# Kernel tuning notes

Hardware: AMD Instinct MI355X
Metric: run time of the kernel (lower is better)

Reference implementation:

```python
import jax, jax.numpy as jnp
import numpy as np

D_MODEL = 512
NHEAD = 8
COORD_DIM = 3
B, N = 2, 2048


def setup_inputs() -> dict:
    key = jax.random.key(0)
    ks = jax.random.split(key, 6)
    x = jax.random.normal(ks[0], (B, N, D_MODEL), dtype=jnp.float32)
    coords = jax.random.normal(ks[1], (B, N, COORD_DIM), dtype=jnp.float32)
    attn_mask = jax.random.normal(ks[2], (N, N), dtype=jnp.float32)
    # qkv Linear(d_model, 3*d_model) with bias
    lim = 1.0 / np.sqrt(D_MODEL)
    qkv_w = jax.random.uniform(ks[3], (3 * D_MODEL, D_MODEL), dtype=jnp.float32, minval=-lim, maxval=lim)
    qkv_b = jax.random.uniform(ks[4], (3 * D_MODEL,), dtype=jnp.float32, minval=-lim, maxval=lim)
    # rel_weight is zeros-init in torch; use small random values for a nontrivial test
    rel_weight = 0.02 * jax.random.normal(ks[5], (NHEAD, COORD_DIM), dtype=jnp.float32)
    return {"x": x, "coords": coords, "attn_mask": attn_mask,
            "qkv_w": qkv_w, "qkv_b": qkv_b, "rel_weight": rel_weight}


def reference(x, coords, attn_mask, qkv_w, qkv_b, rel_weight):
    Bb, Nn, D = x.shape
    H = rel_weight.shape[0]
    hd = D // H
    scale = 1.0 / jnp.sqrt(jnp.asarray(hd, dtype=x.dtype))

    qkv = x @ qkv_w.T + qkv_b                      # [B,N,3D]
    q, k, v = jnp.split(qkv, 3, axis=-1)

    def to_heads(t):
        return t.reshape(Bb, Nn, H, hd).transpose(0, 2, 1, 3)  # [B,H,N,hd]

    qh, kh, vh = to_heads(q), to_heads(k), to_heads(v)

    # per-head scalar projection of coordinates: [B,H,N]
    coord_proj = jnp.einsum('bnc,hc->bhn', coords.astype(jnp.float32), rel_weight).astype(x.dtype)

    # scores with relative-coordinate bias and additive float mask (2d kind)
    scores = jnp.einsum('bhqd,bhkd->bhqk', qh, kh) * scale
    scores = scores + coord_proj[:, :, :, None] - coord_proj[:, :, None, :]
    scores = scores + attn_mask[None, None, :, :]

    attn = jax.nn.softmax(scores, axis=-1)
    yh = jnp.einsum('bhqk,bhkd->bhqd', attn, vh)   # [B,H,N,hd]
    return yh.transpose(0, 2, 1, 3).reshape(Bb, Nn, D)
```

## Files before the change

kernel.cpp:

```cpp
#include <hip/hip_runtime.h>
#include <hip/hip_bf16.h>

typedef __bf16 bf16;
typedef __bf16 bf16x4 __attribute__((ext_vector_type(4)));
typedef __bf16 bf16x8 __attribute__((ext_vector_type(8)));
typedef float floatx4 __attribute__((ext_vector_type(4)));

#define D_MODEL 512
#define NHEAD 8
#define HD 64
#define NB 2
#define NN 2048
#define BH (NB*NHEAD)
#define LOG2E 1.4426950408889634f

__global__ __launch_bounds__(256) void convxw(const float* __restrict__ x,
                                              const float* __restrict__ w,
                                              const float* __restrict__ coords,
                                              const float* __restrict__ rw,
                                              bf16* __restrict__ xb,
                                              bf16* __restrict__ wb,
                                              float* __restrict__ cp) {
    int bid = blockIdx.x;
    if (bid >= 2816) {
        int idx = (bid - 2816) * 256 + threadIdx.x;
        int b = idx >> 11, n = idx & 2047;
        float c0 = coords[idx*3 + 0];
        float c1 = coords[idx*3 + 1];
        float c2 = coords[idx*3 + 2];
        for (int h = 0; h < NHEAD; h++) {
            float v = c0*rw[h*3+0] + c1*rw[h*3+1] + c2*rw[h*3+2];
            cp[(size_t)(b*NHEAD + h)*NN + n] = v * LOG2E;
        }
        return;
    }
    int idx = bid * 256 + threadIdx.x;
    const float* src; bf16* dst; int i4;
    if (idx < 524288) { src = x; dst = xb; i4 = idx; }
    else              { src = w; dst = wb; i4 = idx - 524288; }
    float4 v = *(const float4*)(src + (size_t)i4*4);
    bf16x4 o; o[0] = (bf16)v.x; o[1] = (bf16)v.y; o[2] = (bf16)v.z; o[3] = (bf16)v.w;
    *(bf16x4*)(dst + (size_t)i4*4) = o;
}

__global__ __launch_bounds__(256, 4) void qkv_gemm(const bf16* __restrict__ xb,
                                                   const bf16* __restrict__ wb,
                                                   const float* __restrict__ bias,
                                                   bf16* __restrict__ qb,
                                                   bf16* __restrict__ kb,
                                                   bf16* __restrict__ vtb) {
    __shared__ bf16 smem[64*72 + 128*72];
    bf16 (*Ws)[72] = (bf16(*)[72])smem;
    bf16 (*Xs)[72] = (bf16(*)[72])(smem + 64*72);
    int t = threadIdx.x;
    int w = t >> 6, lane = t & 63, quad = lane >> 4, l15 = lane & 15;
    int blk = blockIdx.x;
    int bf = blk % 24, bm = blk / 24;
    int f0 = bf * 64, m0 = bm * 128;

    floatx4 acc[4][2] = {};
    int wrow = t >> 2, wcol = (t & 3) * 16;
    int xrow = t >> 1, xcol = (t & 1) * 32;

    for (int k0 = 0; k0 < D_MODEL; k0 += 64) {
        __syncthreads();
        {
            const bf16* wsrc = wb + (size_t)(f0 + wrow)*D_MODEL + k0 + wcol;
            *(bf16x8*)&Ws[wrow][wcol]   = *(const bf16x8*)wsrc;
            *(bf16x8*)&Ws[wrow][wcol+8] = *(const bf16x8*)(wsrc + 8);
            const bf16* xsrc = xb + (size_t)(m0 + xrow)*D_MODEL + k0 + xcol;
            *(bf16x8*)&Xs[xrow][xcol]    = *(const bf16x8*)xsrc;
            *(bf16x8*)&Xs[xrow][xcol+8]  = *(const bf16x8*)(xsrc + 8);
            *(bf16x8*)&Xs[xrow][xcol+16] = *(const bf16x8*)(xsrc + 16);
            *(bf16x8*)&Xs[xrow][xcol+24] = *(const bf16x8*)(xsrc + 24);
        }
        __syncthreads();
        for (int kf = 0; kf < 2; kf++) {
            bf16x8 af[4], bx[2];
            for (int fi = 0; fi < 4; fi++)
                af[fi] = *(const bf16x8*)&Ws[fi*16 + l15][kf*32 + quad*8];
            for (int mj = 0; mj < 2; mj++)
                bx[mj] = *(const bf16x8*)&Xs[w*32 + mj*16 + l15][kf*32 + quad*8];
            for (int fi = 0; fi < 4; fi++)
                for (int mj = 0; mj < 2; mj++)
                    acc[fi][mj] = __builtin_amdgcn_mfma_f32_16x16x32_bf16(af[fi], bx[mj], acc[fi][mj], 0, 0, 0);
        }
    }

    int mat = f0 >> 9;
    int h = (f0 >> 6) & 7;
    int b = m0 >> 11;
    int nb = m0 & 2047;
    size_t bho = (size_t)(b*NHEAD + h);
    float4 bs4[4];
    for (int fi = 0; fi < 4; fi++)
        bs4[fi] = *(const float4*)(bias + f0 + fi*16 + quad*4);

    if (mat < 2) {
        bf16* dst = (mat == 0) ? qb : kb;
        float sc = (mat == 0) ? 0.125f * LOG2E : 1.0f;
        for (int fi = 0; fi < 4; fi++) {
            for (int mj = 0; mj < 2; mj++) {
                int n = nb + w*32 + mj*16 + l15;
                bf16x4 pv;
                pv[0] = (bf16)((acc[fi][mj][0] + bs4[fi].x) * sc);
                pv[1] = (bf16)((acc[fi][mj][1] + bs4[fi].y) * sc);
                pv[2] = (bf16)((acc[fi][mj][2] + bs4[fi].z) * sc);
                pv[3] = (bf16)((acc[fi][mj][3] + bs4[fi].w) * sc);
                *(bf16x4*)(dst + (bho*NN + n)*HD + fi*16 + quad*4) = pv;
            }
        }
    } else {
        __syncthreads();
        bf16* Vt = smem;
        for (int fi = 0; fi < 4; fi++) {
            int d = fi*16 + quad*4;
            for (int mj = 0; mj < 2; mj++) {
                int mlc = w*32 + mj*16 + l15;
                Vt[(d+0)*136 + mlc] = (bf16)(acc[fi][mj][0] + bs4[fi].x);
                Vt[(d+1)*136 + mlc] = (bf16)(acc[fi][mj][1] + bs4[fi].y);
                Vt[(d+2)*136 + mlc] = (bf16)(acc[fi][mj][2] + bs4[fi].z);
                Vt[(d+3)*136 + mlc] = (bf16)(acc[fi][mj][3] + bs4[fi].w);
            }
        }
        __syncthreads();
        int d = t >> 2, mc = (t & 3) * 32;
        bf16* gdst = vtb + (bho*HD + d)*NN + nb + mc;
        for (int c = 0; c < 4; c++)
            *(bf16x8*)(gdst + c*8) = *(const bf16x8*)&Vt[d*136 + mc + c*8];
    }
}

__global__ __launch_bounds__(256, 4) void attn(const bf16* __restrict__ qb,
                                               const bf16* __restrict__ kb,
                                               const bf16* __restrict__ vtb,
                                               const float* __restrict__ maskf,
                                               const float* __restrict__ cp,
                                               float* __restrict__ op,
                                               float* __restrict__ ml,
                                               float* __restrict__ out,
                                               int ksplit) {
    __shared__ bf16 Ks[64][72];
    __shared__ bf16 Vts[64][72];
    __shared__ bf16 Ps[64][68];
    int t = threadIdx.x;
    int w = t >> 6, lane = t & 63;
    int quad = lane >> 4, l15 = lane & 15;
    int blk = blockIdx.x;
    int bh = blk & 15;
    int rest = blk >> 4;
    int qt = rest & 31, kp = rest >> 5;
    int q0 = qt * 64;
    int nkeys = NN / ksplit;
    int ntiles = nkeys / 64;
    int kbase = kp * nkeys;
    size_t bhoff = (size_t)bh * (NN * HD);

    bf16x8 aq0, aq1;
    {
        const bf16* qp = qb + bhoff + (size_t)(q0 + w*16 + l15)*HD + quad*8;
        aq0 = *(const bf16x8*)(qp);
        aq1 = *(const bf16x8*)(qp + 32);
    }

    float m_i = -1e30f, l_i = 0.f;
    floatx4 o[4] = {};
    int qrow = q0 + w*16 + l15;
    const float* mrow = maskf + (size_t)qrow * NN;
    const float* cpb = cp + (size_t)bh * NN + kbase;
    int srow = t >> 2, scol = (t & 3) * 16;

    bf16x8 kr0, kr1, vr0, vr1;
    float4 bias4[4];
    {
        const bf16* ks = kb + bhoff + (size_t)(kbase + srow)*HD + scol;
        kr0 = *(const bf16x8*)ks; kr1 = *(const bf16x8*)(ks + 8);
        const bf16* vs = vtb + bhoff + (size_t)srow*NN + kbase + scol;
        vr0 = *(const bf16x8*)vs; vr1 = *(const bf16x8*)(vs + 8);
        for (int j = 0; j < 4; j++) {
            float4 mv = *(const float4*)(mrow + kbase + j*16 + quad*4);
            float4 cv = *(const float4*)(cpb + j*16 + quad*4);
            bias4[j].x = fmaf(mv.x, LOG2E, -cv.x);
            bias4[j].y = fmaf(mv.y, LOG2E, -cv.y);
            bias4[j].z = fmaf(mv.z, LOG2E, -cv.z);
            bias4[j].w = fmaf(mv.w, LOG2E, -cv.w);
        }
    }

    for (int kt = 0; kt < ntiles; kt++) {
        __syncthreads();
        *(bf16x8*)&Ks[srow][scol]      = kr0;
        *(bf16x8*)&Ks[srow][scol + 8]  = kr1;
        *(bf16x8*)&Vts[srow][scol]     = vr0;
        *(bf16x8*)&Vts[srow][scol + 8] = vr1;
        __syncthreads();

        float4 mn4[4];
        bool more = (kt + 1 < ntiles);
        if (more) {
            int kn = kbase + (kt+1)*64;
            const bf16* ks = kb + bhoff + (size_t)(kn + srow)*HD + scol;
            kr0 = *(const bf16x8*)ks; kr1 = *(const bf16x8*)(ks + 8);
            const bf16* vs = vtb + bhoff + (size_t)srow*NN + kn + scol;
            vr0 = *(const bf16x8*)vs; vr1 = *(const bf16x8*)(vs + 8);
            for (int j = 0; j < 4; j++)
                mn4[j] = *(const float4*)(mrow + kn + j*16 + quad*4);
        }

        floatx4 s[4];
        for (int j = 0; j < 4; j++) {
            s[j][0] = bias4[j].x; s[j][1] = bias4[j].y;
            s[j][2] = bias4[j].z; s[j][3] = bias4[j].w;
            bf16x8 ka0 = *(const bf16x8*)&Ks[j*16 + l15][quad*8];
            bf16x8 ka1 = *(const bf16x8*)&Ks[j*16 + l15][32 + quad*8];
            s[j] = __builtin_amdgcn_mfma_f32_16x16x32_bf16(ka0, aq0, s[j], 0, 0, 0);
            s[j] = __builtin_amdgcn_mfma_f32_16x16x32_bf16(ka1, aq1, s[j], 0, 0, 0);
        }

        float mx = s[0][0];
        for (int j = 0; j < 4; j++)
            for (int r = 0; r < 4; r++) mx = fmaxf(mx, s[j][r]);
        mx = fmaxf(mx, __shfl_xor(mx, 16));
        mx = fmaxf(mx, __shfl_xor(mx, 32));
        float mnew = fmaxf(m_i, mx);
        float al = __builtin_amdgcn_exp2f(m_i - mnew);
        float rs = 0.f;
        for (int j = 0; j < 4; j++)
            for (int r = 0; r < 4; r++) {
                float p = __builtin_amdgcn_exp2f(s[j][r] - mnew);
                s[j][r] = p;
                rs += p;
            }
        rs += __shfl_xor(rs, 16);
        rs += __shfl_xor(rs, 32);
        l_i = l_i * al + rs;
        m_i = mnew;

        float alc[4];
        for (int r = 0; r < 4; r++) alc[r] = __shfl(al, quad*4 + r);
        for (int dj = 0; dj < 4; dj++)
            for (int r = 0; r < 4; r++) o[dj][r] *= alc[r];

        for (int j = 0; j < 4; j++) {
            bf16x4 pv;
            pv[0] = (bf16)s[j][0]; pv[1] = (bf16)s[j][1];
            pv[2] = (bf16)s[j][2]; pv[3] = (bf16)s[j][3];
            *(bf16x4*)&Ps[w*16 + l15][j*16 + quad*4] = pv;
        }

        for (int kf2 = 0; kf2 < 2; kf2++) {
            bf16x4 apl = *(const bf16x4*)&Ps[w*16 + l15][kf2*32 + quad*8];
            bf16x4 aph = *(const bf16x4*)&Ps[w*16 + l15][kf2*32 + quad*8 + 4];
            bf16x8 ap;
            ap[0]=apl[0]; ap[1]=apl[1]; ap[2]=apl[2]; ap[3]=apl[3];
            ap[4]=aph[0]; ap[5]=aph[1]; ap[6]=aph[2]; ap[7]=aph[3];
            for (int dj = 0; dj < 4; dj++) {
                bf16x8 bv = *(const bf16x8*)&Vts[dj*16 + l15][kf2*32 + quad*8];
                o[dj] = __builtin_amdgcn_mfma_f32_16x16x32_bf16(ap, bv, o[dj], 0, 0, 0);
            }
        }

        if (more) {
            int kn_loc = (kt+1)*64;
            for (int j = 0; j < 4; j++) {
                float4 cv = *(const float4*)(cpb + kn_loc + j*16 + quad*4);
                bias4[j].x = fmaf(mn4[j].x, LOG2E, -cv.x);
                bias4[j].y = fmaf(mn4[j].y, LOG2E, -cv.y);
                bias4[j].z = fmaf(mn4[j].z, LOG2E, -cv.z);
                bias4[j].w = fmaf(mn4[j].w, LOG2E, -cv.w);
            }
        }
    }

    int b = bh >> 3, h = bh & 7;
    if (ksplit == 1) {
        float lc[4];
        for (int r = 0; r < 4; r++) lc[r] = __shfl(l_i, quad*4 + r);
        for (int dj = 0; dj < 4; dj++) {
            for (int r = 0; r < 4; r++) {
                int n = q0 + w*16 + quad*4 + r;
                out[((size_t)(b*NN + n))*D_MODEL + h*HD + dj*16 + l15] = o[dj][r] / lc[r];
            }
        }
    } else {
        size_t pbase = (size_t)kp * BH * NN;
        for (int dj = 0; dj < 4; dj++) {
            for (int r = 0; r < 4; r++) {
                int n = q0 + w*16 + quad*4 + r;
                op[(pbase + bh*NN + n)*HD + dj*16 + l15] = o[dj][r];
            }
        }
        if (quad == 0) {
            float2 v; v.x = m_i; v.y = l_i;
            *(float2*)(ml + (pbase + (size_t)bh*NN + qrow)*2) = v;
        }
    }
}

__global__ __launch_bounds__(256) void combineN(const float* __restrict__ op,
                                                const float* __restrict__ ml,
                                                float* __restrict__ out,
                                                int ksplit) {
    int idx = blockIdx.x * 256 + threadIdx.x;
    int row = idx >> 4, c4 = (idx & 15) * 4;
    float mstar = -1e30f;
    for (int kp = 0; kp < ksplit; kp++)
        mstar = fmaxf(mstar, ml[((size_t)kp*BH*NN + row)*2]);
    float denom = 0.f;
    float ax = 0.f, ay = 0.f, az = 0.f, aw = 0.f;
    for (int kp = 0; kp < ksplit; kp++) {
        float2 m2 = *(const float2*)(ml + ((size_t)kp*BH*NN + row)*2);
        float wgt = __builtin_amdgcn_exp2f(m2.x - mstar);
        denom += wgt * m2.y;
        float4 ov = *(const float4*)(op + ((size_t)kp*BH*NN + row)*HD + c4);
        ax += wgt*ov.x; ay += wgt*ov.y; az += wgt*ov.z; aw += wgt*ov.w;
    }
    float inv = 1.0f / denom;
    int bh = row >> 11, q = row & 2047;
    int b = bh >> 3, h = bh & 7;
    float4 res; res.x = ax*inv; res.y = ay*inv; res.z = az*inv; res.w = aw*inv;
    *(float4*)(out + ((size_t)(b*NN + q))*D_MODEL + h*HD + c4) = res;
}

extern "C" void kernel_launch(void* const* d_in, const int* in_sizes, int n_in,
                              void* d_out, int out_size, void* d_ws, size_t ws_size,
                              hipStream_t stream) {
    const float* x      = (const float*)d_in[0];
    const float* coords = (const float*)d_in[1];
    const float* amask  = (const float*)d_in[2];
    const float* qkv_w  = (const float*)d_in[3];
    const float* qkv_b  = (const float*)d_in[4];
    const float* rw     = (const float*)d_in[5];
    float* out = (float*)d_out;

    char* ws = (char*)d_ws;
    float* cp  = (float*)(ws + 0);
    bf16*  xb  = (bf16*) (ws + 131072);
    bf16*  wb  = (bf16*) (ws + 4325376);
    bf16*  qb  = (bf16*) (ws + 5898240);
    bf16*  kb  = (bf16*) (ws + 10092544);
    bf16*  vtb = (bf16*) (ws + 14286848);
    float* op  = (float*)(ws + 18481152);

    int split = 1;
    if (ws_size >= 53084160u)      split = 4;
    else if (ws_size >= 35782656u) split = 2;
    float* ml = (float*)(ws + 18481152 + (size_t)split*8388608);

    convxw   <<<dim3(2832), dim3(256), 0, stream>>>(x, qkv_w, coords, rw, xb, wb, cp);
    qkv_gemm <<<dim3(768),  dim3(256), 0, stream>>>(xb, wb, qkv_b, qb, kb, vtb);
    attn     <<<dim3(512*split), dim3(256), 0, stream>>>(qb, kb, vtb, amask, cp, op, ml, out, split);
    if (split > 1)
        combineN<<<dim3(2048), dim3(256), 0, stream>>>(op, ml, out, split);
}
```

Baseline: 155.7 us.

## Remap attention blocks across XCDs, skip unneeded rescale, prefetch coord bias early

Changes the block-to-work mapping so consecutive block IDs, which the hardware spreads round-robin across the 8 XCDs, group by key split and query tile per XCD. This is meant to improve L2 locality of K/V and mask reads. It also skips the online-softmax rescale of the output accumulator whenever no row max increased in the wave, and issues the next tile's coord-projection loads with the other prefetches instead of after the PV MMAs. The remap assumes the grid size divides cleanly into the XCD scheme for every ksplit value. The conditional rescale adds a wave-level vote branch.

```diff
diff --git a/kernel.cpp b/kernel.cpp
--- a/kernel.cpp
+++ b/kernel.cpp
@@ -147,9 +147,16 @@
     int w = t >> 6, lane = t & 63;
     int quad = lane >> 4, l15 = lane & 15;
     int blk = blockIdx.x;
-    int bh = blk & 15;
-    int rest = blk >> 4;
-    int qt = rest & 31, kp = rest >> 5;
+
+    int ls = (ksplit == 4) ? 2 : (ksplit == 2) ? 1 : 0;
+    int shift = 3 - ls;
+    int xcd = blk & 7;
+    int rest = blk >> 3;
+    int bh = rest & 15;
+    int hi = rest >> 4;
+    int kp = xcd >> shift;
+    int qt = (hi << shift) | (xcd & ((1 << shift) - 1));
+
     int q0 = qt * 64;
     int nkeys = NN / ksplit;
     int ntiles = nkeys / 64;
@@ -195,7 +202,7 @@
         *(bf16x8*)&Vts[srow][scol + 8] = vr1;
         __syncthreads();
 
-        float4 mn4[4];
+        float4 mn4[4], cvn[4];
         bool more = (kt + 1 < ntiles);
         if (more) {
             int kn = kbase + (kt+1)*64;
@@ -203,8 +210,11 @@
             kr0 = *(const bf16x8*)ks; kr1 = *(const bf16x8*)(ks + 8);
             const bf16* vs = vtb + bhoff + (size_t)srow*NN + kn + scol;
             vr0 = *(const bf16x8*)vs; vr1 = *(const bf16x8*)(vs + 8);
-            for (int j = 0; j < 4; j++)
+            int knl = (kt+1)*64;
+            for (int j = 0; j < 4; j++) {
                 mn4[j] = *(const float4*)(mrow + kn + j*16 + quad*4);
+                cvn[j] = *(const float4*)(cpb + knl + j*16 + quad*4);
+            }
         }
 
         floatx4 s[4];
@@ -222,24 +232,28 @@
             for (int r = 0; r < 4; r++) mx = fmaxf(mx, s[j][r]);
         mx = fmaxf(mx, __shfl_xor(mx, 16));
         mx = fmaxf(mx, __shfl_xor(mx, 32));
-        float mnew = fmaxf(m_i, mx);
-        float al = __builtin_amdgcn_exp2f(m_i - mnew);
+
+        if (!__all(mx <= m_i)) {
+            float mnew = fmaxf(m_i, mx);
+            float al = __builtin_amdgcn_exp2f(m_i - mnew);
+            l_i *= al;
+            float alc[4];
+            for (int r = 0; r < 4; r++) alc[r] = __shfl(al, quad*4 + r);
+            for (int dj = 0; dj < 4; dj++)
+                for (int r = 0; r < 4; r++) o[dj][r] *= alc[r];
+            m_i = mnew;
+        }
+
         float rs = 0.f;
         for (int j = 0; j < 4; j++)
             for (int r = 0; r < 4; r++) {
-                float p = __builtin_amdgcn_exp2f(s[j][r] - mnew);
+                float p = __builtin_amdgcn_exp2f(s[j][r] - m_i);
                 s[j][r] = p;
                 rs += p;
             }
         rs += __shfl_xor(rs, 16);
         rs += __shfl_xor(rs, 32);
-        l_i = l_i * al + rs;
-        m_i = mnew;
-
-        float alc[4];
-        for (int r = 0; r < 4; r++) alc[r] = __shfl(al, quad*4 + r);
-        for (int dj = 0; dj < 4; dj++)
-            for (int r = 0; r < 4; r++) o[dj][r] *= alc[r];
+        l_i += rs;
 
         for (int j = 0; j < 4; j++) {
             bf16x4 pv;
@@ -261,13 +275,11 @@
         }
 
         if (more) {
-            int kn_loc = (kt+1)*64;
             for (int j = 0; j < 4; j++) {
-                float4 cv = *(const float4*)(cpb + kn_loc + j*16 + quad*4);
-                bias4[j].x = fmaf(mn4[j].x, LOG2E, -cv.x);
-                bias4[j].y = fmaf(mn4[j].y, LOG2E, -cv.y);
-                bias4[j].z = fmaf(mn4[j].z, LOG2E, -cv.z);
-                bias4[j].w = fmaf(mn4[j].w, LOG2E, -cv.w);
+                bias4[j].x = fmaf(mn4[j].x, LOG2E, -cvn[j].x);
+                bias4[j].y = fmaf(mn4[j].y, LOG2E, -cvn[j].y);
+                bias4[j].z = fmaf(mn4[j].z, LOG2E, -cvn[j].z);
+                bias4[j].w = fmaf(mn4[j].w, LOG2E, -cvn[j].w);
             }
         }
     }
```

New measurement: 164.8 us. +5.8%, slower.

## Process two query sub-tiles per attention block to reuse K/V tiles

Applied to the files above, without the earlier changes.

Each attention block now handles 128 query rows as two 64-row halves that share every K/V tile staged in LDS, which halves K/V global traffic and the block count. The coordinate projection for the key range is cached in shared memory. The online-softmax rescale is skipped when no row max increases. Partial outputs are written with nontemporal stores. The cost is more registers, so the occupancy hint drops from 4 to 3 blocks, and the grid shrinks, which may underfill the GPU.

```diff
diff --git a/kernel.cpp b/kernel.cpp
--- a/kernel.cpp
+++ b/kernel.cpp
@@ -131,7 +131,7 @@
     }
 }
 
-__global__ __launch_bounds__(256, 4) void attn(const bf16* __restrict__ qb,
+__global__ __launch_bounds__(256, 3) void attn(const bf16* __restrict__ qb,
                                                const bf16* __restrict__ kb,
                                                const bf16* __restrict__ vtb,
                                                const float* __restrict__ maskf,
@@ -143,48 +143,61 @@
     __shared__ bf16 Ks[64][72];
     __shared__ bf16 Vts[64][72];
     __shared__ bf16 Ps[64][68];
+    __shared__ float Cs[2048];
     int t = threadIdx.x;
     int w = t >> 6, lane = t & 63;
     int quad = lane >> 4, l15 = lane & 15;
     int blk = blockIdx.x;
     int bh = blk & 15;
     int rest = blk >> 4;
-    int qt = rest & 31, kp = rest >> 5;
-    int q0 = qt * 64;
+    int qt = rest & 15, kp = rest >> 4;
+    int q0 = qt * 128;
     int nkeys = NN / ksplit;
     int ntiles = nkeys / 64;
     int kbase = kp * nkeys;
     size_t bhoff = (size_t)bh * (NN * HD);
 
-    bf16x8 aq0, aq1;
+    bf16x8 aqA0, aqA1, aqB0, aqB1;
     {
         const bf16* qp = qb + bhoff + (size_t)(q0 + w*16 + l15)*HD + quad*8;
-        aq0 = *(const bf16x8*)(qp);
-        aq1 = *(const bf16x8*)(qp + 32);
-    }
-
-    float m_i = -1e30f, l_i = 0.f;
-    floatx4 o[4] = {};
+        aqA0 = *(const bf16x8*)(qp);
+        aqA1 = *(const bf16x8*)(qp + 32);
+        aqB0 = *(const bf16x8*)(qp + 64*HD);
+        aqB1 = *(const bf16x8*)(qp + 64*HD + 32);
+    }
+
+    float mA = -1e30f, lA = 0.f, mB = -1e30f, lB = 0.f;
+    floatx4 oA[4] = {}, oB[4] = {};
     int qrow = q0 + w*16 + l15;
-    const float* mrow = maskf + (size_t)qrow * NN;
-    const float* cpb = cp + (size_t)bh * NN + kbase;
+    const float* mrowA = maskf + (size_t)qrow * NN;
+    const float* mrowB = mrowA + (size_t)64 * NN;
+    const float* cpb = cp + (size_t)bh * NN;
     int srow = t >> 2, scol = (t & 3) * 16;
 
+    for (int i = t; i < nkeys; i += 256) Cs[i] = cpb[kbase + i];
+
     bf16x8 kr0, kr1, vr0, vr1;
-    float4 bias4[4];
     {
         const bf16* ks = kb + bhoff + (size_t)(kbase + srow)*HD + scol;
         kr0 = *(const bf16x8*)ks; kr1 = *(const bf16x8*)(ks + 8);
         const bf16* vs = vtb + bhoff + (size_t)srow*NN + kbase + scol;
         vr0 = *(const bf16x8*)vs; vr1 = *(const bf16x8*)(vs + 8);
-        for (int j = 0; j < 4; j++) {
-            float4 mv = *(const float4*)(mrow + kbase + j*16 + quad*4);
-            float4 cv = *(const float4*)(cpb + j*16 + quad*4);
-            bias4[j].x = fmaf(mv.x, LOG2E, -cv.x);
-            bias4[j].y = fmaf(mv.y, LOG2E, -cv.y);
-            bias4[j].z = fmaf(mv.z, LOG2E, -cv.z);
-            bias4[j].w = fmaf(mv.w, LOG2E, -cv.w);
-        }
+    }
+    __syncthreads();
+
+    float4 biasA[4], biasB[4];
+    for (int j = 0; j < 4; j++) {
+        float4 cv = *(const float4*)&Cs[j*16 + quad*4];
+        float4 va = *(const float4*)(mrowA + kbase + j*16 + quad*4);
+        float4 vb = *(const float4*)(mrowB + kbase + j*16 + quad*4);
+        biasA[j].x = fmaf(va.x, LOG2E, -cv.x);
+        biasA[j].y = fmaf(va.y, LOG2E, -cv.y);
+        biasA[j].z = fmaf(va.z, LOG2E, -cv.z);
+        biasA[j].w = fmaf(va.w, LOG2E, -cv.w);
+        biasB[j].x = fmaf(vb.x, LOG2E, -cv.x);
+        biasB[j].y = fmaf(vb.y, LOG2E, -cv.y);
+        biasB[j].z = fmaf(vb.z, LOG2E, -cv.z);
+        biasB[j].w = fmaf(vb.w, LOG2E, -cv.w);
     }
 
     for (int kt = 0; kt < ntiles; kt++) {
@@ -195,91 +208,157 @@
         *(bf16x8*)&Vts[srow][scol + 8] = vr1;
         __syncthreads();
 
-        float4 mn4[4];
+        float4 mnA[4], mnB[4];
         bool more = (kt + 1 < ntiles);
+        int knl = (kt+1)*64;
         if (more) {
-            int kn = kbase + (kt+1)*64;
+            int kn = kbase + knl;
             const bf16* ks = kb + bhoff + (size_t)(kn + srow)*HD + scol;
             kr0 = *(const bf16x8*)ks; kr1 = *(const bf16x8*)(ks + 8);
             const bf16* vs = vtb + bhoff + (size_t)srow*NN + kn + scol;
             vr0 = *(const bf16x8*)vs; vr1 = *(const bf16x8*)(vs + 8);
+            for (int j = 0; j < 4; j++) {
+                mnA[j] = *(const float4*)(mrowA + kn + j*16 + quad*4);
+                mnB[j] = *(const float4*)(mrowB + kn + j*16 + quad*4);
+            }
+        }
+
+        {
+            floatx4 s[4];
+            for (int j = 0; j < 4; j++) {
+                s[j][0] = biasA[j].x; s[j][1] = biasA[j].y;
+                s[j][2] = biasA[j].z; s[j][3] = biasA[j].w;
+                bf16x8 ka0 = *(const bf16x8*)&Ks[j*16 + l15][quad*8];
+                bf16x8 ka1 = *(const bf16x8*)&Ks[j*16 + l15][32 + quad*8];
+                s[j] = __builtin_amdgcn_mfma_f32_16x16x32_bf16(ka0, aqA0, s[j], 0, 0, 0);
+                s[j] = __builtin_amdgcn_mfma_f32_16x16x32_bf16(ka1, aqA1, s[j], 0, 0, 0);
+            }
+            float mx = s[0][0];
             for (int j = 0; j < 4; j++)
-                mn4[j] = *(const float4*)(mrow + kn + j*16 + quad*4);
-        }
-
-        floatx4 s[4];
-        for (int j = 0; j < 4; j++) {
-            s[j][0] = bias4[j].x; s[j][1] = bias4[j].y;
-            s[j][2] = bias4[j].z; s[j][3] = bias4[j].w;
-            bf16x8 ka0 = *(const bf16x8*)&Ks[j*16 + l15][quad*8];
-            bf16x8 ka1 = *(const bf16x8*)&Ks[j*16 + l15][32 + quad*8];
-            s[j] = __builtin_amdgcn_mfma_f32_16x16x32_bf16(ka0, aq0, s[j], 0, 0, 0);
-            s[j] = __builtin_amdgcn_mfma_f32_16x16x32_bf16(ka1, aq1, s[j], 0, 0, 0);
-        }
-
-        float mx = s[0][0];
-        for (int j = 0; j < 4; j++)
-            for (int r = 0; r < 4; r++) mx = fmaxf(mx, s[j][r]);
-        mx = fmaxf(mx, __shfl_xor(mx, 16));
-        mx = fmaxf(mx, __shfl_xor(mx, 32));
-        float mnew = fmaxf(m_i, mx);
-        float al = __builtin_amdgcn_exp2f(m_i - mnew);
-        float rs = 0.f;
-        for (int j = 0; j < 4; j++)
-            for (int r = 0; r < 4; r++) {
-                float p = __builtin_amdgcn_exp2f(s[j][r] - mnew);
-                s[j][r] = p;
-                rs += p;
-            }
-        rs += __shfl_xor(rs, 16);
-        rs += __shfl_xor(rs, 32);
-        l_i = l_i * al + rs;
-        m_i = mnew;
-
-        float alc[4];
-        for (int r = 0; r < 4; r++) alc[r] = __shfl(al, quad*4 + r);
-        for (int dj = 0; dj < 4; dj++)
-            for (int r = 0; r < 4; r++) o[dj][r] *= alc[r];
-
-        for (int j = 0; j < 4; j++) {
-            bf16x4 pv;
-            pv[0] = (bf16)s[j][0]; pv[1] = (bf16)s[j][1];
-            pv[2] = (bf16)s[j][2]; pv[3] = (bf16)s[j][3];
-            *(bf16x4*)&Ps[w*16 + l15][j*16 + quad*4] = pv;
-        }
-
-        for (int kf2 = 0; kf2 < 2; kf2++) {
-            bf16x4 apl = *(const bf16x4*)&Ps[w*16 + l15][kf2*32 + quad*8];
-            bf16x4 aph = *(const bf16x4*)&Ps[w*16 + l15][kf2*32 + quad*8 + 4];
-            bf16x8 ap;
-            ap[0]=apl[0]; ap[1]=apl[1]; ap[2]=apl[2]; ap[3]=apl[3];
-            ap[4]=aph[0]; ap[5]=aph[1]; ap[6]=aph[2]; ap[7]=aph[3];
-            for (int dj = 0; dj < 4; dj++) {
-                bf16x8 bv = *(const bf16x8*)&Vts[dj*16 + l15][kf2*32 + quad*8];
-                o[dj] = __builtin_amdgcn_mfma_f32_16x16x32_bf16(ap, bv, o[dj], 0, 0, 0);
-            }
-        }
-
+                for (int r = 0; r < 4; r++) mx = fmaxf(mx, s[j][r]);
+            mx = fmaxf(mx, __shfl_xor(mx, 16));
+            mx = fmaxf(mx, __shfl_xor(mx, 32));
+            if (!__all(mx <= mA)) {
+                float mnew = fmaxf(mA, mx);
+                float al = __builtin_amdgcn_exp2f(mA - mnew);
+                lA *= al;
+                float alc[4];
+                for (int r = 0; r < 4; r++) alc[r] = __shfl(al, quad*4 + r);
+                for (int dj = 0; dj < 4; dj++)
+                    for (int r = 0; r < 4; r++) oA[dj][r] *= alc[r];
+                mA = mnew;
+            }
+            float rs = 0.f;
+            for (int j = 0; j < 4; j++)
+                for (int r = 0; r < 4; r++) {
+                    float p = __builtin_amdgcn_exp2f(s[j][r] - mA);
+                    s[j][r] = p;
+                    rs += p;
+                }
+            rs += __shfl_xor(rs, 16);
+            rs += __shfl_xor(rs, 32);
+            lA += rs;
+            for (int j = 0; j < 4; j++) {
+                bf16x4 pv;
+                pv[0] = (bf16)s[j][0]; pv[1] = (bf16)s[j][1];
+                pv[2] = (bf16)s[j][2]; pv[3] = (bf16)s[j][3];
+                *(bf16x4*)&Ps[w*16 + l15][j*16 + quad*4] = pv;
+            }
+            for (int kf2 = 0; kf2 < 2; kf2++) {
+                bf16x4 apl = *(const bf16x4*)&Ps[w*16 + l15][kf2*32 + quad*8];
+                bf16x4 aph = *(const bf16x4*)&Ps[w*16 + l15][kf2*32 + quad*8 + 4];
+                bf16x8 ap;
+                ap[0]=apl[0]; ap[1]=apl[1]; ap[2]=apl[2]; ap[3]=apl[3];
+                ap[4]=aph[0]; ap[5]=aph[1]; ap[6]=aph[2]; ap[7]=aph[3];
+                for (int dj = 0; dj < 4; dj++) {
+                    bf16x8 bv = *(const bf16x8*)&Vts[dj*16 + l15][kf2*32 + quad*8];
+                    oA[dj] = __builtin_amdgcn_mfma_f32_16x16x32_bf16(ap, bv, oA[dj], 0, 0, 0);
+                }
+            }
+        }
         if (more) {
-            int kn_loc = (kt+1)*64;
-            for (int j = 0; j < 4; j++) {
-                float4 cv = *(const float4*)(cpb + kn_loc + j*16 + quad*4);
-                bias4[j].x = fmaf(mn4[j].x, LOG2E, -cv.x);
-                bias4[j].y = fmaf(mn4[j].y, LOG2E, -cv.y);
-                bias4[j].z = fmaf(mn4[j].z, LOG2E, -cv.z);
-                bias4[j].w = fmaf(mn4[j].w, LOG2E, -cv.w);
+            for (int j = 0; j < 4; j++) {
+                float4 cv = *(const float4*)&Cs[knl + j*16 + quad*4];
+                biasA[j].x = fmaf(mnA[j].x, LOG2E, -cv.x);
+                biasA[j].y = fmaf(mnA[j].y, LOG2E, -cv.y);
+                biasA[j].z = fmaf(mnA[j].z, LOG2E, -cv.z);
+                biasA[j].w = fmaf(mnA[j].w, LOG2E, -cv.w);
+            }
+        }
+
+        {
+            floatx4 s[4];
+            for (int j = 0; j < 4; j++) {
+                s[j][0] = biasB[j].x; s[j][1] = biasB[j].y;
+                s[j][2] = biasB[j].z; s[j][3] = biasB[j].w;
+                bf16x8 ka0 = *(const bf16x8*)&Ks[j*16 + l15][quad*8];
+                bf16x8 ka1 = *(const bf16x8*)&Ks[j*16 + l15][32 + quad*8];
+                s[j] = __builtin_amdgcn_mfma_f32_16x16x32_bf16(ka0, aqB0, s[j], 0, 0, 0);
+                s[j] = __builtin_amdgcn_mfma_f32_16x16x32_bf16(ka1, aqB1, s[j], 0, 0, 0);
+            }
+            float mx = s[0][0];
+            for (int j = 0; j < 4; j++)
+                for (int r = 0; r < 4; r++) mx = fmaxf(mx, s[j][r]);
+            mx = fmaxf(mx, __shfl_xor(mx, 16));
+            mx = fmaxf(mx, __shfl_xor(mx, 32));
+            if (!__all(mx <= mB)) {
+                float mnew = fmaxf(mB, mx);
+                float al = __builtin_amdgcn_exp2f(mB - mnew);
+                lB *= al;
+                float alc[4];
+                for (int r = 0; r < 4; r++) alc[r] = __shfl(al, quad*4 + r);
+                for (int dj = 0; dj < 4; dj++)
+                    for (int r = 0; r < 4; r++) oB[dj][r] *= alc[r];
+                mB = mnew;
+            }
+            float rs = 0.f;
+            for (int j = 0; j < 4; j++)
+                for (int r = 0; r < 4; r++) {
+                    float p = __builtin_amdgcn_exp2f(s[j][r] - mB);
+                    s[j][r] = p;
+                    rs += p;
+                }
+            rs += __shfl_xor(rs, 16);
+            rs += __shfl_xor(rs, 32);
+            lB += rs;
+            for (int j = 0; j < 4; j++) {
+                bf16x4 pv;
+                pv[0] = (bf16)s[j][0]; pv[1] = (bf16)s[j][1];
+                pv[2] = (bf16)s[j][2]; pv[3] = (bf16)s[j][3];
+                *(bf16x4*)&Ps[w*16 + l15][j*16 + quad*4] = pv;
+            }
+            for (int kf2 = 0; kf2 < 2; kf2++) {
+                bf16x4 apl = *(const bf16x4*)&Ps[w*16 + l15][kf2*32 + quad*8];
+                bf16x4 aph = *(const bf16x4*)&Ps[w*16 + l15][kf2*32 + quad*8 + 4];
+                bf16x8 ap;
+                ap[0]=apl[0]; ap[1]=apl[1]; ap[2]=apl[2]; ap[3]=apl[3];
+                ap[4]=aph[0]; ap[5]=aph[1]; ap[6]=aph[2]; ap[7]=aph[3];
+                for (int dj = 0; dj < 4; dj++) {
+                    bf16x8 bv = *(const bf16x8*)&Vts[dj*16 + l15][kf2*32 + quad*8];
+                    oB[dj] = __builtin_amdgcn_mfma_f32_16x16x32_bf16(ap, bv, oB[dj], 0, 0, 0);
+                }
+            }
+        }
+        if (more) {
+            for (int j = 0; j < 4; j++) {
+                float4 cv = *(const float4*)&Cs[knl + j*16 + quad*4];
+                biasB[j].x = fmaf(mnB[j].x, LOG2E, -cv.x);
+                biasB[j].y = fmaf(mnB[j].y, LOG2E, -cv.y);
+                biasB[j].z = fmaf(mnB[j].z, LOG2E, -cv.z);
+                biasB[j].w = fmaf(mnB[j].w, LOG2E, -cv.w);
             }
         }
     }
 
     int b = bh >> 3, h = bh & 7;
     if (ksplit == 1) {
-        float lc[4];
-        for (int r = 0; r < 4; r++) lc[r] = __shfl(l_i, quad*4 + r);
+        float lcA[4], lcB[4];
+        for (int r = 0; r < 4; r++) { lcA[r] = __shfl(lA, quad*4 + r); lcB[r] = __shfl(lB, quad*4 + r); }
         for (int dj = 0; dj < 4; dj++) {
             for (int r = 0; r < 4; r++) {
                 int n = q0 + w*16 + quad*4 + r;
-                out[((size_t)(b*NN + n))*D_MODEL + h*HD + dj*16 + l15] = o[dj][r] / lc[r];
+                out[((size_t)(b*NN + n))*D_MODEL + h*HD + dj*16 + l15] = oA[dj][r] / lcA[r];
+                out[((size_t)(b*NN + n + 64))*D_MODEL + h*HD + dj*16 + l15] = oB[dj][r] / lcB[r];
             }
         }
     } else {
@@ -287,12 +366,16 @@
         for (int dj = 0; dj < 4; dj++) {
             for (int r = 0; r < 4; r++) {
                 int n = q0 + w*16 + quad*4 + r;
-                op[(pbase + bh*NN + n)*HD + dj*16 + l15] = o[dj][r];
+                __builtin_nontemporal_store(oA[dj][r], op + (pbase + bh*NN + n)*HD + dj*16 + l15);
+                __builtin_nontemporal_store(oB[dj][r], op + (pbase + bh*NN + n + 64)*HD + dj*16 + l15);
             }
         }
         if (quad == 0) {
-            float2 v; v.x = m_i; v.y = l_i;
-            *(float2*)(ml + (pbase + (size_t)bh*NN + qrow)*2) = v;
+            size_t mlbase = (pbase + (size_t)bh*NN + qrow)*2;
+            __builtin_nontemporal_store(mA, ml + mlbase);
+            __builtin_nontemporal_store(lA, ml + mlbase + 1);
+            __builtin_nontemporal_store(mB, ml + mlbase + 128);
+            __builtin_nontemporal_store(lB, ml + mlbase + 129);
         }
     }
 }
@@ -349,7 +432,7 @@
 
     convxw   <<<dim3(2832), dim3(256), 0, stream>>>(x, qkv_w, coords, rw, xb, wb, cp);
     qkv_gemm <<<dim3(768),  dim3(256), 0, stream>>>(xb, wb, qkv_b, qb, kb, vtb);
-    attn     <<<dim3(512*split), dim3(256), 0, stream>>>(qb, kb, vtb, amask, cp, op, ml, out, split);
+    attn     <<<dim3(256*split), dim3(256), 0, stream>>>(qb, kb, vtb, amask, cp, op, ml, out, split);
     if (split > 1)
         combineN<<<dim3(2048), dim3(256), 0, stream>>>(op, ml, out, split);
 }
```

Result: slower. 170.8 us (+9.7%).
